# Optimization experiments

Hardware: AMD Instinct MI355X
Metric: run time of the kernel (lower is better)

The kernel has to match this reference:

```python
import jax, jax.numpy as jnp
import numpy as np

N, C, H, W = 8, 512, 64, 64
CI = 256  # inter_channels = C // reduction


def setup_inputs() -> dict:
    key = jax.random.key(0)
    ks = jax.random.split(key, 9)
    std = 0.01
    return {
        "x": jax.random.normal(ks[0], (N, C, H, W), jnp.float32),
        "g_w": jax.random.normal(ks[1], (CI, C), jnp.float32) * std,
        "g_b": jnp.zeros((CI,), jnp.float32),
        "theta_w": jax.random.normal(ks[2], (CI, C), jnp.float32) * std,
        "theta_b": jnp.zeros((CI,), jnp.float32),
        "phi_w": jax.random.normal(ks[3], (CI, C), jnp.float32) * std,
        "phi_b": jnp.zeros((CI,), jnp.float32),
        "out_w": jax.random.normal(ks[4], (C, CI), jnp.float32) * std,
        "out_b": jnp.zeros((C,), jnp.float32),
    }


def _proj(x, w, b):
    # 1x1 conv == channel matmul: [n,c,h,w] x [o,c] -> [n,o,h,w]
    return jnp.einsum('nchw,oc->nohw', x, w) + b[None, :, None, None]


def reference(x, g_w, g_b, theta_w, theta_b, phi_w, phi_b, out_w, out_b):
    n, c, h, w = x.shape
    hw = h * w
    g_x = _proj(x, g_w, g_b).reshape(n, CI, hw).transpose(0, 2, 1)      # [n, hw, ci]
    theta_x = _proj(x, theta_w, theta_b).reshape(n, CI, hw).transpose(0, 2, 1)  # [n, hw, ci]
    phi_x = _proj(x, phi_w, phi_b).reshape(n, CI, hw)                   # [n, ci, hw]
    # embedded_gaussian: scaled dot-product + softmax over last dim
    pw = jnp.einsum('nqc,nck->nqk', theta_x, phi_x) / jnp.sqrt(jnp.float32(CI))
    pw = jax.nn.softmax(pw, axis=-1)                                    # [n, hw, hw]
    y = jnp.einsum('nqk,nkc->nqc', pw, g_x)                             # [n, hw, ci]
    y = y.transpose(0, 2, 1).reshape(n, CI, h, w)
    return x + _proj(y, out_w, out_b)
```

## Files before the change

### kernel.cpp

```cpp
#include <hip/hip_runtime.h>

#define USH unsigned short
#define U8 unsigned char

typedef __attribute__((ext_vector_type(8))) short s16x8;
typedef __attribute__((ext_vector_type(4))) float f32x4;
typedef __attribute__((ext_vector_type(16))) float f32x16;
typedef __attribute__((ext_vector_type(4))) USH u16x4;
typedef __attribute__((ext_vector_type(2))) unsigned u32x2;
typedef __attribute__((ext_vector_type(4))) unsigned u32x4;
typedef __attribute__((ext_vector_type(8))) int i32x8;

static constexpr int HW = 4096;
static constexpr int C  = 512;
static constexpr int CI = 256;
static constexpr int NB = 8;
static constexpr float LOG2E = 1.44269504088896f;

__device__ __forceinline__ USH f2bf(float f) {
  union { float f; unsigned u; } v; v.f = f;
  unsigned r = v.u + 0x7FFFu + ((v.u >> 16) & 1u);
  return (USH)(r >> 16);
}

__device__ __forceinline__ void mfma_bf16(f32x4& d, s16x8 a, s16x8 b) {
  d = __builtin_amdgcn_mfma_f32_16x16x32_bf16(a, b, d, 0, 0, 0);
}

__device__ __forceinline__ unsigned cvt_fp8x2(float a, float b) {
  unsigned r = 0;
  asm("v_cvt_pk_fp8_f32 %0, %1, %2" : "+v"(r) : "v"(a), "v"(b));
  return r;
}

__device__ __forceinline__ float vexp2(float x) {
  float r;
  asm("v_exp_f32 %0, %1" : "=v"(r) : "v"(x));
  return r;
}

__device__ __forceinline__ void mfma_qk(f32x16& d, i32x8 a, i32x8 b) {
  d = __builtin_amdgcn_mfma_scale_f32_32x32x64_f8f6f4(
      a, b, d, 0 , 0 ,
      0, 0x7f7f7f7f, 0, 0x7b7b7b7b);
}

__device__ __forceinline__ void mfma_pv(f32x16& d, i32x8 a, i32x8 b) {
  d = __builtin_amdgcn_mfma_scale_f32_32x32x64_f8f6f4(
      a, b, d, 0, 0, 0, 0x7f7f7f7f, 0, 0x7f7f7f7f);
}

__device__ __forceinline__ i32x8 pack8(u32x4 a, u32x4 b) {
  i32x8 r = {(int)a.x, (int)a.y, (int)a.z, (int)a.w,
             (int)b.x, (int)b.y, (int)b.z, (int)b.w};
  return r;
}

__device__ __forceinline__ void gload_lds16(const void* g, void* l) {
  __builtin_amdgcn_global_load_lds(
      (__attribute__((address_space(1))) void*)g,
      (__attribute__((address_space(3))) void*)l, 16, 0, 0);
}

__device__ __forceinline__ int swap34(int x) {
  return (x & ~24) | ((x & 8) << 1) | ((x & 16) >> 1);
}

__global__ void conv_w_kernel(const float* __restrict__ th_w, const float* __restrict__ ph_w,
                              const float* __restrict__ g_w, const float* __restrict__ ow,
                              const float* __restrict__ th_b, const float* __restrict__ ph_b,
                              const float* __restrict__ g_b,
                              USH* __restrict__ Wb, USH* __restrict__ OWb,
                              float* __restrict__ b768) {
  int i = blockIdx.x * 256 + threadIdx.x;
  if (i < 768 * 512) {
    int o = i >> 9, c = i & 511;
    float v = (o < 256) ? th_w[o * 512 + c]
            : (o < 512) ? ph_w[(o - 256) * 512 + c]
                        : g_w[(o - 512) * 512 + c];
    Wb[i] = f2bf(v);
  } else {
    int j = i - 768 * 512;
    int c = j >> 9, col = j & 511;
    OWb[j] = f2bf(ow[c * 256 + (col & 255)]);
  }
  if (i < 768) {
    b768[i] = (i < 256) ? th_b[i] : (i < 512) ? ph_b[i - 256] : g_b[i - 512];
  }
}

__global__ __launch_bounds__(256) void xpose_kernel(const float* __restrict__ x,
                                                    USH* __restrict__ Xbt) {
  __shared__ float tile[64][65];
  const int n = blockIdx.z, c0 = blockIdx.y * 64, q0 = blockIdx.x * 64;
  const int t = threadIdx.x;
  const int tq = t & 63, tg = t >> 6;
  const float* src = x + ((size_t)n * C + c0) * HW + q0;
  #pragma unroll
  for (int i = 0; i < 16; i++) {
    int cl = tg + i * 4;
    tile[cl][tq] = src[(size_t)cl * HW + tq];
  }
  __syncthreads();
  USH* dst = Xbt + ((size_t)n * HW + q0) * C + c0;
  #pragma unroll
  for (int i = 0; i < 16; i++) {
    int ql = tg + i * 4;
    dst[(size_t)ql * C + tq] = f2bf(tile[tq][ql]);
  }
}

template <int MODE>
__global__ __launch_bounds__(256, 2) void gemm_bt_kernel(
    const USH* __restrict__ Aall, const USH* __restrict__ Ball,
    U8* __restrict__ q8, U8* __restrict__ k8, U8* __restrict__ v8,
    const float* __restrict__ b768, const float* __restrict__ lsp,
    float* __restrict__ outp, const float* __restrict__ xin, const float* __restrict__ outb) {
  constexpr int KT = 512;
  __shared__ __align__(16) USH As[128 * 64];
  __shared__ __align__(16) USH Bs[128 * 64];
  const int n = blockIdx.z;
  const int m0 = blockIdx.y * 128, n0 = blockIdx.x * 128;
  const USH* A = (MODE == 0) ? Aall + (size_t)n * HW * 512 : Aall;
  const USH* B = (MODE == 0) ? Ball : Ball + (size_t)n * HW * 512;
  const int t = threadIdx.x, L = t & 63, wid = t >> 6;
  const int wm = wid >> 1, wn = wid & 1;
  const int lg = L >> 4, ll = L & 15;
  const int srow = t >> 3, sunit = t & 7;

  f32x4 acc[4][4];
  #pragma unroll
  for (int i = 0; i < 4; i++)
    #pragma unroll
    for (int j = 0; j < 4; j++) acc[i][j] = (f32x4){0.f, 0.f, 0.f, 0.f};

  for (int kt = 0; kt < KT; kt += 64) {
    #pragma unroll
    for (int rnd = 0; rnd < 4; rnd++) {
      int row = srow + rnd * 32;
      int su = sunit ^ (row & 7);
      gload_lds16(A + (size_t)(m0 + row) * KT + kt + su * 8, &As[(rnd * 256 + t) * 8]);
    }
    #pragma unroll
    for (int rnd = 0; rnd < 4; rnd++) {
      int row = srow + rnd * 32;
      int su = sunit ^ (row & 7);
      gload_lds16(B + (size_t)(n0 + row) * KT + kt + su * 8, &Bs[(rnd * 256 + t) * 8]);
    }
    __syncthreads();
    #pragma unroll
    for (int kk = 0; kk < 2; kk++) {
      s16x8 af[4], bf[4];
      #pragma unroll
      for (int mf = 0; mf < 4; mf++) {
        int row = wm * 64 + mf * 16 + ll;
        int u = (kk * 4 + lg) ^ (row & 7);
        af[mf] = *(const s16x8*)&As[row * 64 + u * 8];
      }
      #pragma unroll
      for (int nf = 0; nf < 4; nf++) {
        int row = wn * 64 + nf * 16 + ll;
        int u = (kk * 4 + lg) ^ (row & 7);
        bf[nf] = *(const s16x8*)&Bs[row * 64 + u * 8];
      }
      #pragma unroll
      for (int mf = 0; mf < 4; mf++)
        #pragma unroll
        for (int nf = 0; nf < 4; nf++) mfma_bf16(acc[mf][nf], af[mf], bf[nf]);
    }
    __syncthreads();
  }

  if constexpr (MODE == 0) {
    const int region = n0 >> 8;
    #pragma unroll
    for (int mf = 0; mf < 4; mf++) {
      int q = m0 + wm * 64 + mf * 16 + lg * 4;
      #pragma unroll
      for (int nf = 0; nf < 4; nf++) {
        int o = n0 + wn * 64 + nf * 16 + ll;
        float bia = b768[o];
        if (region == 2) {
          int op = o - 512;
          unsigned w = cvt_fp8x2(acc[mf][nf][0] + bia, acc[mf][nf][1] + bia)
                     | (cvt_fp8x2(acc[mf][nf][2] + bia, acc[mf][nf][3] + bia) << 16);
          int qk = swap34(q);
          *(unsigned*)&v8[((size_t)n * CI + op) * HW + qk] = w;
        } else {
          U8* dst = (region == 0) ? q8 : k8;
          float scl = (region == 0) ? LOG2E : 1.0f;
          int po = swap34(o & 255);
          #pragma unroll
          for (int r = 0; r < 4; r++) {
            unsigned w = cvt_fp8x2((acc[mf][nf][r] + bia) * scl, 0.f);
            dst[((size_t)n * HW + q + r) * 256 + po] = (U8)(w & 255u);
          }
        }
      }
    }
  } else {
    #pragma unroll
    for (int mf = 0; mf < 4; mf++) {
      int c = m0 + wm * 64 + mf * 16 + lg * 4;
      #pragma unroll
      for (int nf = 0; nf < 4; nf++) {
        int q = n0 + wn * 64 + nf * 16 + ll;
        float iv = 1.0f / (lsp[(size_t)n * HW + q] + lsp[32768 + (size_t)n * HW + q]);
        #pragma unroll
        for (int r = 0; r < 4; r++) {
          size_t idx = ((size_t)n * C + c + r) * HW + q;
          outp[idx] = acc[mf][nf][r] * iv + outb[c + r] + xin[idx];
        }
      }
    }
  }
}

__global__ __launch_bounds__(256, 2) void flash11_kernel(
    const U8* __restrict__ Qf, const U8* __restrict__ Kf,
    const U8* __restrict__ Vf, USH* __restrict__ Pa, float* __restrict__ lsp) {
  __shared__ __align__(16) char lds[73728];
  const int n = blockIdx.x;
  const int q0 = blockIdx.y * 128;
  const int kh = blockIdx.z;
  const int t = threadIdx.x;
  const int L = t & 63, wid = t >> 6;
  const int qsub = wid;
  const int lm = L & 31, hi = L >> 5;

  u32x4 qf[8];
  {
    const U8* qr = Qf + (((size_t)n * HW) + q0 + qsub * 32 + lm) * 256 + hi * 32;
    #pragma unroll
    for (int i = 0; i < 8; ++i) qf[i] = *(const u32x4*)(qr + (i >> 1) * 64 + (i & 1) * 16);
  }

  const int prow = ((lm & ~12) | ((lm & 4) << 1) | ((lm & 8) >> 1));
  int koff[8];
  #pragma unroll
  for (int c = 0; c < 4; ++c) {
    koff[2 * c]     = prow * 256 + (((4 * c + 2 * hi)     ^ (prow & 15)) * 16);
    koff[2 * c + 1] = prow * 256 + (((4 * c + 2 * hi + 1) ^ (prow & 15)) * 16);
  }

  const U8* kb = Kf + (size_t)n * HW * 256 + (size_t)kh * 2048 * 256;
  const U8* ks[4];
  int kd[4];
  #pragma unroll
  for (int u = 0; u < 4; ++u) {
    int i = u * 256 + t;
    int kr = i >> 4, ku = i & 15;
    ks[u] = kb + kr * 256 + ((ku ^ (kr & 15)) * 16);
    kd[u] = i * 16;
  }

  const U8* vbg = Vf + (size_t)n * CI * HW + kh * 2048;
  const U8* vs[4];
  int vd[4];
  #pragma unroll
  for (int u = 0; u < 4; ++u) {
    int i = u * 256 + t;
    int vr = i >> 2, vu = i & 3;
    vs[u] = vbg + (size_t)vr * HW + vu * 16;
    vd[u] = 32768 + vr * 80 + vu * 16;
  }

  f32x16 O[8];
  #pragma unroll
  for (int i = 0; i < 8; ++i)
    #pragma unroll
    for (int j = 0; j < 16; ++j) O[i][j] = 0.f;
  float lsum = 0.f;

  #pragma unroll
  for (int u = 0; u < 4; ++u) { gload_lds16(ks[u], lds + kd[u]); ks[u] += 16384; }
  u32x4 vreg[4];
  #pragma unroll
  for (int u = 0; u < 4; ++u) { vreg[u] = *(const u32x4*)vs[u]; vs[u] += 64; }

  for (int s = 0; s < 32; ++s) {
    asm volatile("s_waitcnt vmcnt(0)" ::: "memory");
    const int vbo = (s & 1) * 20480;
    #pragma unroll
    for (int u = 0; u < 4; ++u) *(u32x4*)(lds + vbo + vd[u]) = vreg[u];
    if (s < 31) {
      #pragma unroll
      for (int u = 0; u < 4; ++u) { vreg[u] = *(const u32x4*)vs[u]; vs[u] += 64; }
    }
    asm volatile("s_waitcnt lgkmcnt(0)" ::: "memory");
    __builtin_amdgcn_s_barrier();
    if (s < 31) {
      const int ko = ((s + 1) & 1) * 16384;
      #pragma unroll
      for (int u = 0; u < 4; ++u) { gload_lds16(ks[u], lds + ko + kd[u]); ks[u] += 16384; }
    }
    const char* kslot = lds + (s & 1) * 16384;
    const char* vb = lds + 32768 + vbo;
    __builtin_amdgcn_s_setprio(1);
    unsigned pw[8];
    #pragma unroll
    for (int s2 = 0; s2 < 2; ++s2) {
      f32x16 S;
      #pragma unroll
      for (int j = 0; j < 16; ++j) S[j] = 0.f;
      #pragma unroll
      for (int c = 0; c < 4; ++c) {
        u32x4 a0 = *(const u32x4*)(kslot + s2 * 8192 + koff[2 * c]);
        u32x4 a1 = *(const u32x4*)(kslot + s2 * 8192 + koff[2 * c + 1]);
        mfma_qk(S, pack8(a0, a1), pack8(qf[2 * c], qf[2 * c + 1]));
      }
      float p[16];
      #pragma unroll
      for (int r = 0; r < 16; ++r) p[r] = vexp2(S[r]);
      {
        float s0 = (p[0] + p[1]) + (p[2] + p[3]);
        float s1 = (p[4] + p[5]) + (p[6] + p[7]);
        float s2s = (p[8] + p[9]) + (p[10] + p[11]);
        float s3 = (p[12] + p[13]) + (p[14] + p[15]);
        lsum += (s0 + s1) + (s2s + s3);
      }
      pw[4 * s2 + 0] = cvt_fp8x2(p[0], p[1]) | (cvt_fp8x2(p[2], p[3]) << 16);
      pw[4 * s2 + 1] = cvt_fp8x2(p[4], p[5]) | (cvt_fp8x2(p[6], p[7]) << 16);
      pw[4 * s2 + 2] = cvt_fp8x2(p[8], p[9]) | (cvt_fp8x2(p[10], p[11]) << 16);
      pw[4 * s2 + 3] = cvt_fp8x2(p[12], p[13]) | (cvt_fp8x2(p[14], p[15]) << 16);
    }
    i32x8 pa = {(int)pw[0], (int)pw[1], (int)pw[2], (int)pw[3],
                (int)pw[4], (int)pw[5], (int)pw[6], (int)pw[7]};
    #pragma unroll
    for (int g = 0; g < 8; ++g) {
      const char* vr = vb + (g * 32 + lm) * 80;
      u32x4 v0 = *(const u32x4*)(vr + hi * 16);
      u32x4 v1 = *(const u32x4*)(vr + 32 + hi * 16);
      mfma_pv(O[g], pa, pack8(v0, v1));
    }
    __builtin_amdgcn_s_setprio(0);
  }

  lsum += __shfl_xor(lsum, 32);
  if (L < 32)
    lsp[(size_t)kh * 32768 + (size_t)n * HW + q0 + qsub * 32 + lm] = lsum;
  USH* pw2 = Pa + ((size_t)n * HW + q0 + qsub * 32) * 512 + kh * 256 + lm;
  #pragma unroll
  for (int g = 0; g < 8; ++g)
    #pragma unroll
    for (int r = 0; r < 16; ++r) {
      int qr = (r & 3) + 8 * (r >> 2) + 4 * hi;
      pw2[(size_t)qr * 512 + g * 32] = f2bf(O[g][r]);
    }
}

extern "C" void kernel_launch(void* const* d_in, const int* in_sizes, int n_in,
                              void* d_out, int out_size, void* d_ws, size_t ws_size,
                              hipStream_t stream) {
  (void)in_sizes; (void)n_in; (void)out_size; (void)ws_size;
  const float* x    = (const float*)d_in[0];
  const float* g_w  = (const float*)d_in[1];
  const float* g_b  = (const float*)d_in[2];
  const float* th_w = (const float*)d_in[3];
  const float* th_b = (const float*)d_in[4];
  const float* ph_w = (const float*)d_in[5];
  const float* ph_b = (const float*)d_in[6];
  const float* ow   = (const float*)d_in[7];
  const float* ob   = (const float*)d_in[8];

  U8* Qf = (U8*)d_out;
  U8* Kf = Qf + (size_t)NB * HW * CI;
  U8* Vf = Kf + (size_t)NB * HW * CI;

  char* w = (char*)d_ws;
  USH* Xbt = (USH*)w;
  USH* Pa  = Xbt;
  USH* Wb  = (USH*)(w + 33554432);
  USH* OWb = (USH*)(w + 34340864);
  float* b768 = (float*)(w + 34865152);
  float* lsp  = (float*)(w + 34869248);

  conv_w_kernel<<<2560, 256, 0, stream>>>(th_w, ph_w, g_w, ow, th_b, ph_b, g_b, Wb, OWb, b768);
  xpose_kernel<<<dim3(64, 8, 8), 256, 0, stream>>>(x, Xbt);
  gemm_bt_kernel<0><<<dim3(6, 32, 8), 256, 0, stream>>>(Xbt, Wb, Qf, Kf, Vf, b768,
                                                        nullptr, nullptr, nullptr, nullptr);
  flash11_kernel<<<dim3(8, 32, 2), 256, 0, stream>>>(Qf, Kf, Vf, Pa, lsp);
  gemm_bt_kernel<1><<<dim3(32, 4, 8), 256, 0, stream>>>(OWb, (const USH*)Pa,
                                                        nullptr, nullptr, nullptr,
                                                        nullptr, lsp, (float*)d_out, x, ob);
}
```

Before: 172.5 us.

## Convert projection GEMMs and intermediates from bf16 to scaled fp8 MX MFMA

```diff
diff --git a/kernel.cpp b/kernel.cpp
--- a/kernel.cpp
+++ b/kernel.cpp
@@ -3,11 +3,7 @@
 #define USH unsigned short
 #define U8 unsigned char
 
-typedef __attribute__((ext_vector_type(8))) short s16x8;
-typedef __attribute__((ext_vector_type(4))) float f32x4;
 typedef __attribute__((ext_vector_type(16))) float f32x16;
-typedef __attribute__((ext_vector_type(4))) USH u16x4;
-typedef __attribute__((ext_vector_type(2))) unsigned u32x2;
 typedef __attribute__((ext_vector_type(4))) unsigned u32x4;
 typedef __attribute__((ext_vector_type(8))) int i32x8;
 
@@ -17,37 +13,25 @@
 static constexpr int NB = 8;
 static constexpr float LOG2E = 1.44269504088896f;
 
-__device__ __forceinline__ USH f2bf(float f) {
-  union { float f; unsigned u; } v; v.f = f;
-  unsigned r = v.u + 0x7FFFu + ((v.u >> 16) & 1u);
-  return (USH)(r >> 16);
-}
-
-__device__ __forceinline__ void mfma_bf16(f32x4& d, s16x8 a, s16x8 b) {
-  d = __builtin_amdgcn_mfma_f32_16x16x32_bf16(a, b, d, 0, 0, 0);
-}
-
 __device__ __forceinline__ unsigned cvt_fp8x2(float a, float b) {
   unsigned r = 0;
   asm("v_cvt_pk_fp8_f32 %0, %1, %2" : "+v"(r) : "v"(a), "v"(b));
   return r;
 }
 
+__device__ __forceinline__ U8 fp8b(float v) {
+  return (U8)(cvt_fp8x2(v, 0.f) & 255u);
+}
+
 __device__ __forceinline__ float vexp2(float x) {
   float r;
   asm("v_exp_f32 %0, %1" : "=v"(r) : "v"(x));
   return r;
 }
 
-__device__ __forceinline__ void mfma_qk(f32x16& d, i32x8 a, i32x8 b) {
-  d = __builtin_amdgcn_mfma_scale_f32_32x32x64_f8f6f4(
-      a, b, d, 0 , 0 ,
-      0, 0x7f7f7f7f, 0, 0x7b7b7b7b);
-}
-
-__device__ __forceinline__ void mfma_pv(f32x16& d, i32x8 a, i32x8 b) {
-  d = __builtin_amdgcn_mfma_scale_f32_32x32x64_f8f6f4(
-      a, b, d, 0, 0, 0, 0x7f7f7f7f, 0, 0x7f7f7f7f);
+template <unsigned SA, unsigned SB>
+__device__ __forceinline__ void mfma_mx(f32x16& d, i32x8 a, i32x8 b) {
+  d = __builtin_amdgcn_mfma_scale_f32_32x32x64_f8f6f4(a, b, d, 0, 0, 0, SA, 0, SB);
 }
 
 __device__ __forceinline__ i32x8 pack8(u32x4 a, u32x4 b) {
@@ -70,7 +54,7 @@
                               const float* __restrict__ g_w, const float* __restrict__ ow,
                               const float* __restrict__ th_b, const float* __restrict__ ph_b,
                               const float* __restrict__ g_b,
-                              USH* __restrict__ Wb, USH* __restrict__ OWb,
+                              U8* __restrict__ W8, U8* __restrict__ OW8,
                               float* __restrict__ b768) {
   int i = blockIdx.x * 256 + threadIdx.x;
   if (i < 768 * 512) {
@@ -78,19 +62,19 @@
     float v = (o < 256) ? th_w[o * 512 + c]
             : (o < 512) ? ph_w[(o - 256) * 512 + c]
                         : g_w[(o - 512) * 512 + c];
-    Wb[i] = f2bf(v);
+    W8[i] = fp8b(v * 64.f);
   } else {
     int j = i - 768 * 512;
     int c = j >> 9, col = j & 511;
-    OWb[j] = f2bf(ow[c * 256 + (col & 255)]);
+    OW8[j] = fp8b(ow[c * 256 + (col & 255)] * 64.f);
   }
   if (i < 768) {
     b768[i] = (i < 256) ? th_b[i] : (i < 512) ? ph_b[i - 256] : g_b[i - 512];
   }
 }
 
-__global__ __launch_bounds__(256) void xpose_kernel(const float* __restrict__ x,
-                                                    USH* __restrict__ Xbt) {
+__global__ __launch_bounds__(256) void xpose8_kernel(const float* __restrict__ x,
+                                                     U8* __restrict__ x8t) {
   __shared__ float tile[64][65];
   const int n = blockIdx.z, c0 = blockIdx.y * 64, q0 = blockIdx.x * 64;
   const int t = threadIdx.x;
@@ -102,123 +86,131 @@
     tile[cl][tq] = src[(size_t)cl * HW + tq];
   }
   __syncthreads();
-  USH* dst = Xbt + ((size_t)n * HW + q0) * C + c0;
-  #pragma unroll
-  for (int i = 0; i < 16; i++) {
-    int ql = tg + i * 4;
-    dst[(size_t)ql * C + tq] = f2bf(tile[tq][ql]);
+  const int c4 = (t & 15) * 4, qb = (t >> 4) * 4;
+  U8* dst = x8t + ((size_t)n * HW + q0) * C + c0 + c4;
+  #pragma unroll
+  for (int j = 0; j < 4; j++) {
+    int q = qb + j;
+    unsigned w = cvt_fp8x2(tile[c4][q], tile[c4 + 1][q])
+               | (cvt_fp8x2(tile[c4 + 2][q], tile[c4 + 3][q]) << 16);
+    *(unsigned*)&dst[(size_t)q * C] = w;
   }
 }
 
 template <int MODE>
-__global__ __launch_bounds__(256, 2) void gemm_bt_kernel(
-    const USH* __restrict__ Aall, const USH* __restrict__ Ball,
+__global__ __launch_bounds__(256, 2) void gemm_mx_kernel(
+    const U8* __restrict__ Aall, const U8* __restrict__ Ball,
     U8* __restrict__ q8, U8* __restrict__ k8, U8* __restrict__ v8,
     const float* __restrict__ b768, const float* __restrict__ lsp,
     float* __restrict__ outp, const float* __restrict__ xin, const float* __restrict__ outb) {
-  constexpr int KT = 512;
-  __shared__ __align__(16) USH As[128 * 64];
-  __shared__ __align__(16) USH Bs[128 * 64];
+  __shared__ __align__(16) U8 As[8192];
+  __shared__ __align__(16) U8 Bs[8192];
   const int n = blockIdx.z;
   const int m0 = blockIdx.y * 128, n0 = blockIdx.x * 128;
-  const USH* A = (MODE == 0) ? Aall + (size_t)n * HW * 512 : Aall;
-  const USH* B = (MODE == 0) ? Ball : Ball + (size_t)n * HW * 512;
+  const U8* A = (MODE == 0) ? Aall + (size_t)n * HW * 512 : Aall;
+  const U8* B = (MODE == 0) ? Ball : Ball + (size_t)n * HW * 512;
   const int t = threadIdx.x, L = t & 63, wid = t >> 6;
   const int wm = wid >> 1, wn = wid & 1;
-  const int lg = L >> 4, ll = L & 15;
-  const int srow = t >> 3, sunit = t & 7;
-
-  f32x4 acc[4][4];
-  #pragma unroll
-  for (int i = 0; i < 4; i++)
-    #pragma unroll
-    for (int j = 0; j < 4; j++) acc[i][j] = (f32x4){0.f, 0.f, 0.f, 0.f};
-
-  for (int kt = 0; kt < KT; kt += 64) {
-    #pragma unroll
-    for (int rnd = 0; rnd < 4; rnd++) {
-      int row = srow + rnd * 32;
-      int su = sunit ^ (row & 7);
-      gload_lds16(A + (size_t)(m0 + row) * KT + kt + su * 8, &As[(rnd * 256 + t) * 8]);
-    }
-    #pragma unroll
-    for (int rnd = 0; rnd < 4; rnd++) {
-      int row = srow + rnd * 32;
-      int su = sunit ^ (row & 7);
-      gload_lds16(B + (size_t)(n0 + row) * KT + kt + su * 8, &Bs[(rnd * 256 + t) * 8]);
-    }
+  const int lm = L & 31, hi = L >> 5;
+
+  f32x16 acc[2][2];
+  #pragma unroll
+  for (int i = 0; i < 2; i++)
+    #pragma unroll
+    for (int j = 0; j < 2; j++)
+      #pragma unroll
+      for (int e = 0; e < 16; e++) acc[i][j][e] = 0.f;
+
+  const int r0 = t >> 2, u0 = (t & 3) ^ ((r0 >> 1) & 3);
+  const int r1 = (t + 256) >> 2, u1 = (t & 3) ^ ((r1 >> 1) & 3);
+  const int d0 = t * 16, d1 = (t + 256) * 16;
+
+  for (int kt = 0; kt < 512; kt += 64) {
+    gload_lds16(A + (size_t)(m0 + r0) * 512 + kt + u0 * 16, As + d0);
+    gload_lds16(A + (size_t)(m0 + r1) * 512 + kt + u1 * 16, As + d1);
+    gload_lds16(B + (size_t)(n0 + r0) * 512 + kt + u0 * 16, Bs + d0);
+    gload_lds16(B + (size_t)(n0 + r1) * 512 + kt + u1 * 16, Bs + d1);
     __syncthreads();
-    #pragma unroll
-    for (int kk = 0; kk < 2; kk++) {
-      s16x8 af[4], bf[4];
-      #pragma unroll
-      for (int mf = 0; mf < 4; mf++) {
-        int row = wm * 64 + mf * 16 + ll;
-        int u = (kk * 4 + lg) ^ (row & 7);
-        af[mf] = *(const s16x8*)&As[row * 64 + u * 8];
-      }
-      #pragma unroll
-      for (int nf = 0; nf < 4; nf++) {
-        int row = wn * 64 + nf * 16 + ll;
-        int u = (kk * 4 + lg) ^ (row & 7);
-        bf[nf] = *(const s16x8*)&Bs[row * 64 + u * 8];
-      }
-      #pragma unroll
-      for (int mf = 0; mf < 4; mf++)
-        #pragma unroll
-        for (int nf = 0; nf < 4; nf++) mfma_bf16(acc[mf][nf], af[mf], bf[nf]);
-    }
+    i32x8 af[2], bf[2];
+    #pragma unroll
+    for (int mi = 0; mi < 2; ++mi) {
+      int row = wm * 64 + mi * 32 + lm;
+      int f = (row >> 1) & 3;
+      u32x4 a0 = *(const u32x4*)(As + row * 64 + ((2 * hi) ^ f) * 16);
+      u32x4 a1 = *(const u32x4*)(As + row * 64 + ((2 * hi + 1) ^ f) * 16);
+      af[mi] = pack8(a0, a1);
+    }
+    #pragma unroll
+    for (int ni = 0; ni < 2; ++ni) {
+      int row = wn * 64 + ni * 32 + lm;
+      int f = (row >> 1) & 3;
+      u32x4 b0 = *(const u32x4*)(Bs + row * 64 + ((2 * hi) ^ f) * 16);
+      u32x4 b1 = *(const u32x4*)(Bs + row * 64 + ((2 * hi + 1) ^ f) * 16);
+      bf[ni] = pack8(b0, b1);
+    }
+    #pragma unroll
+    for (int mi = 0; mi < 2; ++mi)
+      #pragma unroll
+      for (int ni = 0; ni < 2; ++ni) {
+        if constexpr (MODE == 0)
+          mfma_mx<0x7f7f7f7fu, 0x79797979u>(acc[mi][ni], af[mi], bf[ni]);
+        else
+          mfma_mx<0x79797979u, 0x83838383u>(acc[mi][ni], af[mi], bf[ni]);
+      }
     __syncthreads();
   }
 
   if constexpr (MODE == 0) {
     const int region = n0 >> 8;
     #pragma unroll
-    for (int mf = 0; mf < 4; mf++) {
-      int q = m0 + wm * 64 + mf * 16 + lg * 4;
-      #pragma unroll
-      for (int nf = 0; nf < 4; nf++) {
-        int o = n0 + wn * 64 + nf * 16 + ll;
-        float bia = b768[o];
+    for (int ni = 0; ni < 2; ++ni) {
+      const int o = n0 + wn * 64 + ni * 32 + lm;
+      const float bia = b768[o];
+      #pragma unroll
+      for (int mi = 0; mi < 2; ++mi) {
+        const int qb = m0 + wm * 64 + mi * 32 + 4 * hi;
         if (region == 2) {
-          int op = o - 512;
-          unsigned w = cvt_fp8x2(acc[mf][nf][0] + bia, acc[mf][nf][1] + bia)
-                     | (cvt_fp8x2(acc[mf][nf][2] + bia, acc[mf][nf][3] + bia) << 16);
-          int qk = swap34(q);
-          *(unsigned*)&v8[((size_t)n * CI + op) * HW + qk] = w;
+          const int op = o - 512;
+          #pragma unroll
+          for (int rb = 0; rb < 4; ++rb) {
+            unsigned w =
+                cvt_fp8x2(acc[mi][ni][4 * rb] + bia, acc[mi][ni][4 * rb + 1] + bia)
+              | (cvt_fp8x2(acc[mi][ni][4 * rb + 2] + bia, acc[mi][ni][4 * rb + 3] + bia) << 16);
+            *(unsigned*)&v8[((size_t)n * CI + op) * HW + swap34(qb + 8 * rb)] = w;
+          }
         } else {
           U8* dst = (region == 0) ? q8 : k8;
-          float scl = (region == 0) ? LOG2E : 1.0f;
-          int po = swap34(o & 255);
+          const float scl = (region == 0) ? LOG2E : 1.0f;
+          const int po = swap34(o & 255);
           #pragma unroll
-          for (int r = 0; r < 4; r++) {
-            unsigned w = cvt_fp8x2((acc[mf][nf][r] + bia) * scl, 0.f);
-            dst[((size_t)n * HW + q + r) * 256 + po] = (U8)(w & 255u);
+          for (int r = 0; r < 16; ++r) {
+            int q = qb + (r & 3) + 8 * (r >> 2);
+            dst[((size_t)n * HW + q) * 256 + po] = fp8b((acc[mi][ni][r] + bia) * scl);
           }
         }
       }
     }
   } else {
     #pragma unroll
-    for (int mf = 0; mf < 4; mf++) {
-      int c = m0 + wm * 64 + mf * 16 + lg * 4;
-      #pragma unroll
-      for (int nf = 0; nf < 4; nf++) {
-        int q = n0 + wn * 64 + nf * 16 + ll;
-        float iv = 1.0f / (lsp[(size_t)n * HW + q] + lsp[32768 + (size_t)n * HW + q]);
+    for (int ni = 0; ni < 2; ++ni) {
+      const int q = n0 + wn * 64 + ni * 32 + lm;
+      const float iv = 1.0f / (lsp[(size_t)n * HW + q] + lsp[32768 + (size_t)n * HW + q]);
+      #pragma unroll
+      for (int mi = 0; mi < 2; ++mi) {
         #pragma unroll
-        for (int r = 0; r < 4; r++) {
-          size_t idx = ((size_t)n * C + c + r) * HW + q;
-          outp[idx] = acc[mf][nf][r] * iv + outb[c + r] + xin[idx];
+        for (int r = 0; r < 16; ++r) {
+          int c = m0 + wm * 64 + mi * 32 + (r & 3) + 8 * (r >> 2) + 4 * hi;
+          size_t idx = ((size_t)n * C + c) * HW + q;
+          outp[idx] = acc[mi][ni][r] * iv + outb[c] + xin[idx];
         }
       }
     }
   }
 }
 
-__global__ __launch_bounds__(256, 2) void flash11_kernel(
+__global__ __launch_bounds__(256, 2) void flash12_kernel(
     const U8* __restrict__ Qf, const U8* __restrict__ Kf,
-    const U8* __restrict__ Vf, USH* __restrict__ Pa, float* __restrict__ lsp) {
+    const U8* __restrict__ Vf, U8* __restrict__ Pa8, float* __restrict__ lsp) {
   __shared__ __align__(16) char lds[73728];
   const int n = blockIdx.x;
   const int q0 = blockIdx.y * 128;
@@ -307,7 +299,7 @@
       for (int c = 0; c < 4; ++c) {
         u32x4 a0 = *(const u32x4*)(kslot + s2 * 8192 + koff[2 * c]);
         u32x4 a1 = *(const u32x4*)(kslot + s2 * 8192 + koff[2 * c + 1]);
-        mfma_qk(S, pack8(a0, a1), pack8(qf[2 * c], qf[2 * c + 1]));
+        mfma_mx<0x7f7f7f7fu, 0x7b7b7b7bu>(S, pack8(a0, a1), pack8(qf[2 * c], qf[2 * c + 1]));
       }
       float p[16];
       #pragma unroll
@@ -331,7 +323,7 @@
       const char* vr = vb + (g * 32 + lm) * 80;
       u32x4 v0 = *(const u32x4*)(vr + hi * 16);
       u32x4 v1 = *(const u32x4*)(vr + 32 + hi * 16);
-      mfma_pv(O[g], pa, pack8(v0, v1));
+      mfma_mx<0x7f7f7f7fu, 0x7f7f7f7fu>(O[g], pa, pack8(v0, v1));
     }
     __builtin_amdgcn_s_setprio(0);
   }
@@ -339,13 +331,13 @@
   lsum += __shfl_xor(lsum, 32);
   if (L < 32)
     lsp[(size_t)kh * 32768 + (size_t)n * HW + q0 + qsub * 32 + lm] = lsum;
-  USH* pw2 = Pa + ((size_t)n * HW + q0 + qsub * 32) * 512 + kh * 256 + lm;
+  U8* pw2 = Pa8 + ((size_t)n * HW + q0 + qsub * 32) * 512 + kh * 256 + lm;
   #pragma unroll
   for (int g = 0; g < 8; ++g)
     #pragma unroll
     for (int r = 0; r < 16; ++r) {
       int qr = (r & 3) + 8 * (r >> 2) + 4 * hi;
-      pw2[(size_t)qr * 512 + g * 32] = f2bf(O[g][r]);
+      pw2[(size_t)qr * 512 + g * 32] = fp8b(O[g][r] * 0.0625f);
     }
 }
 
@@ -368,19 +360,18 @@
   U8* Vf = Kf + (size_t)NB * HW * CI;
 
   char* w = (char*)d_ws;
-  USH* Xbt = (USH*)w;
-  USH* Pa  = Xbt;
-  USH* Wb  = (USH*)(w + 33554432);
-  USH* OWb = (USH*)(w + 34340864);
-  float* b768 = (float*)(w + 34865152);
-  float* lsp  = (float*)(w + 34869248);
-
-  conv_w_kernel<<<2560, 256, 0, stream>>>(th_w, ph_w, g_w, ow, th_b, ph_b, g_b, Wb, OWb, b768);
-  xpose_kernel<<<dim3(64, 8, 8), 256, 0, stream>>>(x, Xbt);
-  gemm_bt_kernel<0><<<dim3(6, 32, 8), 256, 0, stream>>>(Xbt, Wb, Qf, Kf, Vf, b768,
+  U8* x8t = (U8*)w;
+  U8* Pa8 = x8t;
+  U8* W8  = (U8*)(w + 16777216);
+  U8* OW8 = (U8*)(w + 17170432);
+  float* b768 = (float*)(w + 17432576);
+  float* lsp  = (float*)(w + 17436672);
+
+  conv_w_kernel<<<2560, 256, 0, stream>>>(th_w, ph_w, g_w, ow, th_b, ph_b, g_b, W8, OW8, b768);
+  xpose8_kernel<<<dim3(64, 8, 8), 256, 0, stream>>>(x, x8t);
+  gemm_mx_kernel<0><<<dim3(6, 32, 8), 256, 0, stream>>>(x8t, W8, Qf, Kf, Vf, b768,
                                                         nullptr, nullptr, nullptr, nullptr);
-  flash11_kernel<<<dim3(8, 32, 2), 256, 0, stream>>>(Qf, Kf, Vf, Pa, lsp);
-  gemm_bt_kernel<1><<<dim3(32, 4, 8), 256, 0, stream>>>(OWb, (const USH*)Pa,
-                                                        nullptr, nullptr, nullptr,
+  flash12_kernel<<<dim3(8, 32, 2), 256, 0, stream>>>(Qf, Kf, Vf, Pa8, lsp);
+  gemm_mx_kernel<1><<<dim3(32, 4, 8), 256, 0, stream>>>(OW8, Pa8, nullptr, nullptr, nullptr,
                                                         nullptr, lsp, (float*)d_out, x, ob);
 }
```

Measured after the change: 157.4 us. 8.8% less time.
